# Performance work log

Measured on AMD Instinct MI355X. Metric: run time of the kernel, lower is better.

Reference implementation:

```python
import jax, jax.numpy as jnp
import numpy as np

B, Q, D, H, P, F = 16, 300, 256, 8, 4, 2048
HG = WG = 100          # feature-map height/width (hw = 10000, perfect square)
HW = HG * WG
DH = D // H
EPS = 1e-5


def _ln(x, g, b):
    m = x.mean(-1, keepdims=True)
    v = jnp.var(x, axis=-1, keepdims=True)
    return (x - m) * jax.lax.rsqrt(v + EPS) * g + b


def setup_inputs() -> dict:
    key = jax.random.key(0)
    ks = jax.random.split(key, 24)
    rn = lambda k, shape, s=0.02: jax.random.normal(k, shape, jnp.float32) * s
    return {
        "tgt": jax.random.normal(ks[0], (B, Q, D), jnp.float32),
        "memory": jax.random.normal(ks[1], (B, HW, D), jnp.float32),
        "in_proj_w": rn(ks[2], (D, 3 * D)), "in_proj_b": rn(ks[3], (3 * D,)),
        "out_proj_w": rn(ks[4], (D, D)), "out_proj_b": rn(ks[5], (D,)),
        "norm1_g": jnp.ones((D,), jnp.float32), "norm1_b": jnp.zeros((D,), jnp.float32),
        "ref_w": rn(ks[6], (D, 2)), "ref_b": rn(ks[7], (2,)),
        "off_w": rn(ks[8], (D, H * P * 2)), "off_b": rn(ks[9], (H * P * 2,)),
        "attw_w": rn(ks[10], (D, H * P)), "attw_b": rn(ks[11], (H * P,)),
        "vproj_w": rn(ks[12], (D, D)), "vproj_b": rn(ks[13], (D,)),
        "oproj_w": rn(ks[14], (D, D)), "oproj_b": rn(ks[15], (D,)),
        "norm2_g": jnp.ones((D,), jnp.float32), "norm2_b": jnp.zeros((D,), jnp.float32),
        "lin1_w": rn(ks[16], (D, F)), "lin1_b": rn(ks[17], (F,)),
        "lin2_w": rn(ks[18], (F, D)), "lin2_b": rn(ks[19], (D,)),
        "norm3_g": jnp.ones((D,), jnp.float32), "norm3_b": jnp.zeros((D,), jnp.float32),
    }


def reference(tgt, memory, in_proj_w, in_proj_b, out_proj_w, out_proj_b,
              norm1_g, norm1_b, ref_w, ref_b, off_w, off_b, attw_w, attw_b,
              vproj_w, vproj_b, oproj_w, oproj_b, norm2_g, norm2_b,
              lin1_w, lin1_b, lin2_w, lin2_b, norm3_g, norm3_b):
    # ---- self-attention (nn.MultiheadAttention, eval mode: dropout = identity)
    qkv = tgt @ in_proj_w + in_proj_b                      # [B,Q,3D]
    q, k, v = jnp.split(qkv, 3, axis=-1)
    q = q.reshape(B, Q, H, DH)
    k = k.reshape(B, Q, H, DH)
    v = v.reshape(B, Q, H, DH)
    scores = jnp.einsum('bqhd,bkhd->bhqk', q, k) / jnp.sqrt(jnp.float32(DH))
    attn = jax.nn.softmax(scores, axis=-1)
    sa = jnp.einsum('bhqk,bkhd->bqhd', attn, v).reshape(B, Q, D) @ out_proj_w + out_proj_b
    x = _ln(tgt + sa, norm1_g, norm1_b)

    # ---- reference points
    ref = jax.nn.sigmoid(x @ ref_w + ref_b)                # [B,Q,2] in (0,1)

    # ---- deformable cross-attention
    offs = (x @ off_w + off_b).reshape(B, Q, H, P, 2)
    wts = jax.nn.softmax((x @ attw_w + attw_b).reshape(B, Q, H, P), axis=-1)
    vals = (memory @ vproj_w + vproj_b).reshape(B, HW, H, DH)
    loc = jnp.clip(ref[:, :, None, None, :] + offs, 0.0, 1.0)
    sx = loc[..., 0] * (WG - 1)
    sy = loc[..., 1] * (HG - 1)
    x0 = jnp.floor(sx)
    y0 = jnp.floor(sy)
    x0i = jnp.clip(x0.astype(jnp.int32), 0, WG - 1)
    y0i = jnp.clip(y0.astype(jnp.int32), 0, HG - 1)
    x1i = jnp.clip(x0i + 1, 0, WG - 1)
    y1i = jnp.clip(y0i + 1, 0, HG - 1)
    wx1 = sx - x0
    wx0 = 1.0 - wx1
    wy1 = sy - y0
    wy0 = 1.0 - wy1
    bi = jnp.arange(B)[:, None, None, None]
    hi = jnp.arange(H)[None, None, :, None]

    def gather(yi, xi):                                    # [B,Q,H,P,DH]
        return vals[bi, yi * WG + xi, hi]

    samp = (gather(y0i, x0i) * (wx0 * wy0)[..., None]
            + gather(y1i, x0i) * (wx0 * wy1)[..., None]
            + gather(y0i, x1i) * (wx1 * wy0)[..., None]
            + gather(y1i, x1i) * (wx1 * wy1)[..., None])
    ca = (samp * wts[..., None]).sum(axis=3).reshape(B, Q, D) @ oproj_w + oproj_b
    x = _ln(x + ca, norm2_g, norm2_b)

    # ---- FFN
    ff = jax.nn.relu(x @ lin1_w + lin1_b) @ lin2_w + lin2_b
    return _ln(x + ff, norm3_g, norm3_b)
```

## Files before the change

### kernel.cpp

```cpp
#include <hip/hip_runtime.h>

#define NB   16
#define NQ   300
#define ND   256
#define NH   8
#define NP   4
#define NF   2048
#define NHW  10000
#define NWG  100
#define NROW 4800

typedef __attribute__((ext_vector_type(8))) short bf16x8;
typedef __attribute__((ext_vector_type(4))) float f32x4;

__device__ __forceinline__ unsigned short f2bf(float f) {
    unsigned u = __builtin_bit_cast(unsigned, f);
    u = (u + 0x7fffu + ((u >> 16) & 1u)) >> 16;
    return (unsigned short)u;
}
__device__ __forceinline__ float bf2f(unsigned short h) {
    unsigned u = ((unsigned)h) << 16;
    return __builtin_bit_cast(float, u);
}

__device__ __forceinline__ bf16x8 cvt8(float4 lo, float4 hi) {
    unsigned r0, r1, r2, r3;
    asm("v_cvt_pk_bf16_f32 %0, %1, %2" : "=v"(r0) : "v"(lo.x), "v"(lo.y));
    asm("v_cvt_pk_bf16_f32 %0, %1, %2" : "=v"(r1) : "v"(lo.z), "v"(lo.w));
    asm("v_cvt_pk_bf16_f32 %0, %1, %2" : "=v"(r2) : "v"(hi.x), "v"(hi.y));
    asm("v_cvt_pk_bf16_f32 %0, %1, %2" : "=v"(r3) : "v"(hi.z), "v"(hi.w));
    uint4 u = {r0, r1, r2, r3};
    return __builtin_bit_cast(bf16x8, u);
}

__device__ __forceinline__ void gl_lds16(const unsigned short* g, unsigned short* l) {
    __builtin_amdgcn_global_load_lds(
        (__attribute__((address_space(1))) const void*)g,
        (__attribute__((address_space(3))) void*)l,
        16, 0, 0);
}

__global__ __launch_bounds__(256) void transpose_cast(
    const float* __restrict__ w_in,  const float* __restrict__ w_out,
    const float* __restrict__ w_vp,  const float* __restrict__ w_op,
    const float* __restrict__ w_l1,  const float* __restrict__ w_l2,
    unsigned short* __restrict__ o_in, unsigned short* __restrict__ o_out,
    unsigned short* __restrict__ o_vp, unsigned short* __restrict__ o_op,
    unsigned short* __restrict__ o_l1, unsigned short* __restrict__ o_l2)
{
    __shared__ float ts[64][65];
    int b = blockIdx.x;
    const float* src; unsigned short* dst; int K, N, ncx;
    if      (b < 48)  { src = w_in;  dst = o_in;  K = 256;  N = 768;  ncx = 12; }
    else if (b < 64)  { src = w_out; dst = o_out; K = 256;  N = 256;  ncx = 4;  b -= 48; }
    else if (b < 80)  { src = w_vp;  dst = o_vp;  K = 256;  N = 256;  ncx = 4;  b -= 64; }
    else if (b < 96)  { src = w_op;  dst = o_op;  K = 256;  N = 256;  ncx = 4;  b -= 80; }
    else if (b < 224) { src = w_l1;  dst = o_l1;  K = 256;  N = 2048; ncx = 32; b -= 96; }
    else              { src = w_l2;  dst = o_l2;  K = 2048; N = 256;  ncx = 4;  b -= 224; }
    const int n0 = (b % ncx) * 64, k0 = (b / ncx) * 64;
    const int t = threadIdx.x;
    const int r = t >> 4, c = t & 15;
    #pragma unroll
    for (int j = 0; j < 4; j++) {
        float4 v = *(const float4*)(src + (long)(k0 + j * 16 + r) * N + n0 + c * 4);
        ts[j * 16 + r][c * 4 + 0] = v.x;
        ts[j * 16 + r][c * 4 + 1] = v.y;
        ts[j * 16 + r][c * 4 + 2] = v.z;
        ts[j * 16 + r][c * 4 + 3] = v.w;
    }
    __syncthreads();
    #pragma unroll
    for (int j = 0; j < 4; j++) {
        unsigned short o[4];
        #pragma unroll
        for (int i = 0; i < 4; i++)
            o[i] = f2bf(ts[c * 4 + i][j * 16 + r]);
        *(uint2*)(dst + (long)(n0 + j * 16 + r) * K + k0 + c * 4) = *(uint2*)o;
    }
}

__global__ __launch_bounds__(256) void prep_head(
    const float* __restrict__ rw, const float* __restrict__ rb,
    const float* __restrict__ ow, const float* __restrict__ ob,
    const float* __restrict__ aw, const float* __restrict__ ab,
    unsigned short* __restrict__ o_hd, float* __restrict__ o_hb)
{
    int id = blockIdx.x * 256 + threadIdx.x;
    if (id < 32768) {
        int n = id >> 8, k = id & 255;
        float v;
        if (n < 2)       v = rw[k * 2 + n];
        else if (n < 66) v = ow[k * 64 + (n - 2)];
        else if (n < 98) v = aw[k * 32 + (n - 66)];
        else             v = 0.0f;
        o_hd[id] = f2bf(v);
        return;
    }
    id -= 32768;
    if (id < 128) {
        float v;
        if (id < 2)       v = rb[id];
        else if (id < 66) v = ob[id - 2];
        else if (id < 98) v = ab[id - 66];
        else              v = 0.0f;
        o_hb[id] = v;
    }
}

template <int RELU, int OUTBF, int SPLITK, int TN>
__global__ __launch_bounds__(512, 4) void gemm_bt(
    const float* __restrict__ A, const unsigned short* __restrict__ Bt,
    const float* __restrict__ bias, void* __restrict__ Cout,
    int M, int N, int K)
{
    constexpr int NFB = TN / 16;
    constexpr int WN  = TN / 64;
    constexpr int AI  = WN;

    __shared__ __align__(16) unsigned short As[2][8 * 512];
    __shared__ __align__(16) unsigned short Bs[2][NFB * 512];

    const int t    = threadIdx.x;
    const long m0  = (long)blockIdx.y * 128;
    const int  n0  = blockIdx.x * TN;
    const int  wave = t >> 6, lane = t & 63;
    const int  l16 = lane & 15, quad = lane >> 4;
    const int  wmi = wave / WN, wni = wave % WN;
    const int  wm  = wmi * (AI * 16);
    const int  wn  = wni * 64;
    const int  fA  = wmi * AI;
    const int  fB  = wni * 4;

    f32x4 acc[AI][4] = {};

    const int kChunk = K / SPLITK;
    const int kBeg   = (SPLITK > 1) ? blockIdx.z * kChunk : 0;
    const int nk     = kChunk / 32;

    const long aRow   = m0 + wave * 16 + l16;
    const bool aValid = (aRow < M);
    const float* aP   = A + aRow * (long)K + kBeg + (quad << 3);
    unsigned short* aW = &As[0][(wave << 9) + (lane << 3)];

    const unsigned short* bP;
    unsigned short* bW;
    if constexpr (TN == 256) {
        bP = Bt + (long)(n0 + wave * 32 + l16) * K + kBeg + (quad << 3);
        bW = &Bs[0][wave << 10];
    } else {
        bP = Bt + (long)(n0 + wave * 16 + l16) * K + kBeg + (quad << 3);
        bW = &Bs[0][wave << 9];
    }

    float4 la0 = make_float4(0.f, 0.f, 0.f, 0.f);
    float4 la1 = make_float4(0.f, 0.f, 0.f, 0.f);

    auto loadA = [&](int kt) {
        if (aValid) {
            la0 = *(const float4*)(aP + kt * 32);
            la1 = *(const float4*)(aP + kt * 32 + 4);
        }
    };
    auto writeA = [&](int buf) {
        const bf16x8 v = cvt8(la0, la1);
        *(bf16x8*)(aW + buf * 4096) = v;
    };
    auto issueB = [&](int kt, int buf) {
        if constexpr (TN == 256) {
            gl_lds16(bP + kt * 32,          bW + buf * (NFB * 512));
            gl_lds16(bP + kt * 32 + 16 * (long)K, bW + buf * (NFB * 512) + 512);
        } else {
            gl_lds16(bP + kt * 32,          bW + buf * (NFB * 512));
        }
    };

    issueB(0, 0);
    loadA(0);
    writeA(0);
    __syncthreads();

    for (int kt = 0; kt < nk; kt++) {
        const int cur = kt & 1;
        if (kt + 1 < nk) {
            issueB(kt + 1, cur ^ 1);
            loadA(kt + 1);
        }

        bf16x8 af[AI], bfr[4];
        #pragma unroll
        for (int i = 0; i < AI; i++)
            af[i] = *(const bf16x8*)&As[cur][(fA + i) * 512 + (lane << 3)];
        #pragma unroll
        for (int j = 0; j < 4; j++)
            bfr[j] = *(const bf16x8*)&Bs[cur][(fB + j) * 512 + (lane << 3)];
        #pragma unroll
        for (int i = 0; i < AI; i++)
            #pragma unroll
            for (int j = 0; j < 4; j++)
                acc[i][j] = __builtin_amdgcn_mfma_f32_16x16x32_bf16(
                    bfr[j], af[i], acc[i][j], 0, 0, 0);

        if (kt + 1 < nk) {
            writeA(cur ^ 1);
            __syncthreads();
        }
    }

    float4 bj[4];
    #pragma unroll
    for (int j = 0; j < 4; j++)
        bj[j] = *(const float4*)&bias[n0 + wn + j * 16 + (quad << 2)];

    float* outp = (float*)Cout;
    float bscale = 1.0f;
    if (SPLITK > 1) {
        outp += (size_t)blockIdx.z * M * N;
        bscale = (blockIdx.z == 0) ? 1.0f : 0.0f;
    }

    #pragma unroll
    for (int i = 0; i < AI; i++) {
        const long gr = m0 + wm + i * 16 + l16;
        if (gr < M) {
            #pragma unroll
            for (int j = 0; j < 4; j++) {
                float4 v;
                v.x = acc[i][j][0] + bscale * bj[j].x;
                v.y = acc[i][j][1] + bscale * bj[j].y;
                v.z = acc[i][j][2] + bscale * bj[j].z;
                v.w = acc[i][j][3] + bscale * bj[j].w;
                if (RELU) {
                    v.x = fmaxf(v.x, 0.f); v.y = fmaxf(v.y, 0.f);
                    v.z = fmaxf(v.z, 0.f); v.w = fmaxf(v.w, 0.f);
                }
                const int gc = n0 + wn + j * 16 + (quad << 2);
                if (OUTBF) {
                    unsigned short o[4] = {f2bf(v.x), f2bf(v.y), f2bf(v.z), f2bf(v.w)};
                    *(uint2*)((unsigned short*)Cout + gr * N + gc) = *(uint2*)o;
                } else {
                    *(float4*)(outp + gr * N + gc) = v;
                }
            }
        }
    }
}

__global__ __launch_bounds__(256) void attn_kernel(
    const float* __restrict__ qkv, float* __restrict__ sa)
{
    __shared__ union {
        struct {
            unsigned short Ks[304][40];
            unsigned short Qs[64][40];
        } s;
        unsigned short Ps[4][16][328];
    } u;
    __shared__ unsigned short Vt[32][328];

    const int bh = blockIdx.y;
    const int b  = bh >> 3, h = bh & 7;
    const int q0 = blockIdx.x * 64;
    const int t  = threadIdx.x;

    for (int idx = t; idx < 304 * 8; idx += 256) {
        const int r = idx >> 3, c4 = (idx & 7) << 2;
        if (r < NQ) {
            const float4 kv = *(const float4*)(qkv + ((long)(b * NQ + r)) * 768 + 256 + h * 32 + c4);
            u.s.Ks[r][c4 + 0] = f2bf(kv.x); u.s.Ks[r][c4 + 1] = f2bf(kv.y);
            u.s.Ks[r][c4 + 2] = f2bf(kv.z); u.s.Ks[r][c4 + 3] = f2bf(kv.w);
        } else {
            u.s.Ks[r][c4 + 0] = 0; u.s.Ks[r][c4 + 1] = 0;
            u.s.Ks[r][c4 + 2] = 0; u.s.Ks[r][c4 + 3] = 0;
        }
    }
    for (int idx = t; idx < NQ * 8; idx += 256) {
        const int key = idx >> 3, dq = (idx & 7) << 2;
        const float4 vv = *(const float4*)(qkv + ((long)(b * NQ + key)) * 768 + 512 + h * 32 + dq);
        Vt[dq + 0][key] = f2bf(vv.x); Vt[dq + 1][key] = f2bf(vv.y);
        Vt[dq + 2][key] = f2bf(vv.z); Vt[dq + 3][key] = f2bf(vv.w);
    }
    for (int idx = t; idx < 32 * 20; idx += 256)
        Vt[idx / 20][300 + idx % 20] = 0;
    for (int idx = t; idx < 64 * 8; idx += 256) {
        const int r = idx >> 3, c4 = (idx & 7) << 2;
        const int q = q0 + r;
        if (q < NQ) {
            const float4 qv = *(const float4*)(qkv + ((long)(b * NQ + q)) * 768 + h * 32 + c4);
            u.s.Qs[r][c4 + 0] = f2bf(qv.x); u.s.Qs[r][c4 + 1] = f2bf(qv.y);
            u.s.Qs[r][c4 + 2] = f2bf(qv.z); u.s.Qs[r][c4 + 3] = f2bf(qv.w);
        } else {
            u.s.Qs[r][c4 + 0] = 0; u.s.Qs[r][c4 + 1] = 0;
            u.s.Qs[r][c4 + 2] = 0; u.s.Qs[r][c4 + 3] = 0;
        }
    }
    __syncthreads();

    const int wave = t >> 6, lane = t & 63;
    const int l16 = lane & 15, quad = lane >> 4;
    const float scale = 0.1767766952966369f;

    const bf16x8 aq = *(const bf16x8*)&u.s.Qs[wave * 16 + l16][quad * 8];
    f32x4 sacc[19];
    #pragma unroll
    for (int kt = 0; kt < 19; kt++) {
        const bf16x8 bk = *(const bf16x8*)&u.s.Ks[kt * 16 + l16][quad * 8];
        sacc[kt] = __builtin_amdgcn_mfma_f32_16x16x32_bf16(
            aq, bk, (f32x4){0.f, 0.f, 0.f, 0.f}, 0, 0, 0);
    }

    float inv[4];
    #pragma unroll
    for (int r = 0; r < 4; r++) {
        float m = -1e30f;
        #pragma unroll
        for (int kt = 0; kt < 19; kt++) {
            float s = sacc[kt][r] * scale;
            if (kt == 18 && l16 >= 12) s = -1e30f;
            sacc[kt][r] = s;
            m = fmaxf(m, s);
        }
        m = fmaxf(m, __shfl_xor(m, 1)); m = fmaxf(m, __shfl_xor(m, 2));
        m = fmaxf(m, __shfl_xor(m, 4)); m = fmaxf(m, __shfl_xor(m, 8));
        float sum = 0.f;
        #pragma unroll
        for (int kt = 0; kt < 19; kt++) {
            float p = __expf(sacc[kt][r] - m);
            sacc[kt][r] = p;
            sum += p;
        }
        sum += __shfl_xor(sum, 1); sum += __shfl_xor(sum, 2);
        sum += __shfl_xor(sum, 4); sum += __shfl_xor(sum, 8);
        inv[r] = 1.0f / sum;
    }

    __syncthreads();

    #pragma unroll
    for (int kt = 0; kt < 19; kt++)
        #pragma unroll
        for (int r = 0; r < 4; r++)
            u.Ps[wave][quad * 4 + r][kt * 16 + l16] = f2bf(sacc[kt][r] * inv[r]);
    #pragma unroll
    for (int r = 0; r < 4; r++)
        u.Ps[wave][quad * 4 + r][304 + l16] = 0;

    f32x4 o0 = {0.f, 0.f, 0.f, 0.f}, o1 = {0.f, 0.f, 0.f, 0.f};
    #pragma unroll
    for (int kt = 0; kt < 10; kt++) {
        const bf16x8 ap  = *(const bf16x8*)&u.Ps[wave][l16][kt * 32 + quad * 8];
        const bf16x8 bv0 = *(const bf16x8*)&Vt[l16][kt * 32 + quad * 8];
        const bf16x8 bv1 = *(const bf16x8*)&Vt[16 + l16][kt * 32 + quad * 8];
        o0 = __builtin_amdgcn_mfma_f32_16x16x32_bf16(ap, bv0, o0, 0, 0, 0);
        o1 = __builtin_amdgcn_mfma_f32_16x16x32_bf16(ap, bv1, o1, 0, 0, 0);
    }

    #pragma unroll
    for (int r = 0; r < 4; r++) {
        const int q = q0 + wave * 16 + quad * 4 + r;
        if (q < NQ) {
            float* op = sa + ((long)(b * NQ + q)) * ND + h * 32;
            op[l16]      = o0[r];
            op[16 + l16] = o1[r];
        }
    }
}

template <int NPART>
__global__ __launch_bounds__(256) void residual_ln(
    const float* __restrict__ a, const float* __restrict__ r,
    const float* __restrict__ gam, const float* __restrict__ bet,
    float* __restrict__ out, long pstride)
{
    const int row  = blockIdx.x * 4 + (threadIdx.x >> 6);
    const int lane = threadIdx.x & 63;
    const long base = (long)row * ND + lane * 4;
    float4 av = *(const float4*)(a + base);
    float4 rv = *(const float4*)(r + base);
    #pragma unroll
    for (int z = 1; z < NPART; z++) {
        float4 pv = *(const float4*)(r + z * pstride + base);
        rv.x += pv.x; rv.y += pv.y; rv.z += pv.z; rv.w += pv.w;
    }
    float x0 = av.x + rv.x, x1 = av.y + rv.y, x2 = av.z + rv.z, x3 = av.w + rv.w;
    float s  = x0 + x1 + x2 + x3;
    float s2 = x0 * x0 + x1 * x1 + x2 * x2 + x3 * x3;
    #pragma unroll
    for (int off = 32; off >= 1; off >>= 1) {
        s  += __shfl_xor(s, off);
        s2 += __shfl_xor(s2, off);
    }
    float mean = s * 0.00390625f;
    float var  = s2 * 0.00390625f - mean * mean;
    float rstd = rsqrtf(var + 1e-5f);
    float4 gv = *(const float4*)(gam + lane * 4);
    float4 bv = *(const float4*)(bet + lane * 4);
    float4 o;
    o.x = (x0 - mean) * rstd * gv.x + bv.x;
    o.y = (x1 - mean) * rstd * gv.y + bv.y;
    o.z = (x2 - mean) * rstd * gv.z + bv.z;
    o.w = (x3 - mean) * rstd * gv.w + bv.w;
    *(float4*)(out + base) = o;
}

__global__ __launch_bounds__(256) void meta_kernel(
    const float* __restrict__ res, float* __restrict__ meta)
{
    const int t   = threadIdx.x;
    const int row = blockIdx.x * 8 + (t >> 5);
    const int s   = t & 31;
    const int h   = s >> 2;
    const float* rp = res + (long)row * 128;
    const float rx = 1.f / (1.f + __expf(-rp[0]));
    const float ry = 1.f / (1.f + __expf(-rp[1]));
    const float offx = rp[2 + 2 * s], offy = rp[3 + 2 * s];
    const float a0 = rp[66 + h * 4 + 0], a1 = rp[66 + h * 4 + 1];
    const float a2 = rp[66 + h * 4 + 2], a3 = rp[66 + h * 4 + 3];
    const float mx = fmaxf(fmaxf(a0, a1), fmaxf(a2, a3));
    const float den = __expf(a0 - mx) + __expf(a1 - mx) +
                      __expf(a2 - mx) + __expf(a3 - mx);
    const float awt = __expf(rp[66 + s] - mx) / den;

    const float lx = fminf(fmaxf(rx + offx, 0.f), 1.f) * (NWG - 1);
    const float ly = fminf(fmaxf(ry + offy, 0.f), 1.f) * (NWG - 1);
    const float fx = floorf(lx), fy = floorf(ly);
    int x0 = (int)fx; x0 = min(max(x0, 0), NWG - 1);
    int y0 = (int)fy; y0 = min(max(y0, 0), NWG - 1);
    const int x1 = min(x0 + 1, NWG - 1);
    const int y1 = min(y0 + 1, NWG - 1);
    const float wx1 = lx - fx, wx0 = 1.f - wx1;
    const float wy1 = ly - fy, wy0 = 1.f - wy1;
    float4 m0, m1;
    m0.x = __int_as_float(y0 * NWG + x0);
    m0.y = __int_as_float(y0 * NWG + x1);
    m0.z = __int_as_float(y1 * NWG + x0);
    m0.w = __int_as_float(y1 * NWG + x1);
    m1.x = awt * wx0 * wy0;
    m1.y = awt * wx1 * wy0;
    m1.z = awt * wx0 * wy1;
    m1.w = awt * wx1 * wy1;
    float* mp = meta + (long)row * 256 + s * 8;
    *(float4*)mp       = m0;
    *(float4*)(mp + 4) = m1;
}

__global__ __launch_bounds__(256) void deform_gather(
    const float* __restrict__ meta, const unsigned short* __restrict__ vals,
    float* __restrict__ ca)
{
    const int row = blockIdx.x;
    const int b = row / NQ;
    __shared__ float ms[256];
    const int t = threadIdx.x;
    ms[t] = meta[(long)row * 256 + t];
    __syncthreads();
    const int h = t >> 5, d = t & 31;
    const unsigned short* vb = vals + (long)b * NHW * ND + h * 32 + d;
    float acc = 0.f;
    #pragma unroll
    for (int p = 0; p < NP; p++) {
        const float* mp = ms + h * 32 + p * 8;
        const int i00 = __float_as_int(mp[0]);
        const int i01 = __float_as_int(mp[1]);
        const int i10 = __float_as_int(mp[2]);
        const int i11 = __float_as_int(mp[3]);
        acc += mp[4] * bf2f(vb[(long)i00 * ND]);
        acc += mp[5] * bf2f(vb[(long)i01 * ND]);
        acc += mp[6] * bf2f(vb[(long)i10 * ND]);
        acc += mp[7] * bf2f(vb[(long)i11 * ND]);
    }
    ca[(long)row * ND + t] = acc;
}

extern "C" void kernel_launch(void* const* d_in, const int* in_sizes, int n_in,
                              void* d_out, int out_size, void* d_ws, size_t ws_size,
                              hipStream_t stream)
{
    (void)in_sizes; (void)n_in; (void)out_size; (void)ws_size;
    const float* tgt   = (const float*)d_in[0];
    const float* mem   = (const float*)d_in[1];
    const float* inpw  = (const float*)d_in[2];
    const float* inpb  = (const float*)d_in[3];
    const float* outw  = (const float*)d_in[4];
    const float* outb  = (const float*)d_in[5];
    const float* n1g   = (const float*)d_in[6];
    const float* n1b   = (const float*)d_in[7];
    const float* refw  = (const float*)d_in[8];
    const float* refb  = (const float*)d_in[9];
    const float* offw  = (const float*)d_in[10];
    const float* offb  = (const float*)d_in[11];
    const float* attww = (const float*)d_in[12];
    const float* attwb = (const float*)d_in[13];
    const float* vpw   = (const float*)d_in[14];
    const float* vpb   = (const float*)d_in[15];
    const float* opw   = (const float*)d_in[16];
    const float* opb   = (const float*)d_in[17];
    const float* n2g   = (const float*)d_in[18];
    const float* n2b   = (const float*)d_in[19];
    const float* l1w   = (const float*)d_in[20];
    const float* l1b   = (const float*)d_in[21];
    const float* l2w   = (const float*)d_in[22];
    const float* l2b   = (const float*)d_in[23];
    const float* n3g   = (const float*)d_in[24];
    const float* n3b   = (const float*)d_in[25];
    float* out = (float*)d_out;

    char* p = (char*)d_ws;
    auto alloc = [&](size_t bytes) {
        char* r = p; p += (bytes + 255) & ~(size_t)255; return (void*)r;
    };
    unsigned short* wtIn   = (unsigned short*)alloc(768 * 256 * 2);
    unsigned short* wtOut  = (unsigned short*)alloc(256 * 256 * 2);
    unsigned short* wtVp   = (unsigned short*)alloc(256 * 256 * 2);
    unsigned short* wtOp   = (unsigned short*)alloc(256 * 256 * 2);
    unsigned short* wtL1   = (unsigned short*)alloc(2048 * 256 * 2);
    unsigned short* wtL2   = (unsigned short*)alloc(256 * 2048 * 2);
    unsigned short* wtHead = (unsigned short*)alloc(128 * 256 * 2);
    float*          headb  = (float*)alloc(128 * 4);
    float* qkv  = (float*)alloc((size_t)NROW * 768 * 4);
    float* sa   = (float*)alloc((size_t)NROW * ND * 4);
    float* x1   = (float*)alloc((size_t)NROW * ND * 4);
    float* x2   = (float*)alloc((size_t)NROW * ND * 4);
    float* tmp  = (float*)alloc((size_t)NROW * ND * 4 * 4);
    float* ca   = (float*)alloc((size_t)NROW * ND * 4);
    float* meta = (float*)alloc((size_t)NROW * 256 * 4);
    void* uni = alloc((size_t)NB * NHW * ND * 2);
    unsigned short* vals = (unsigned short*)uni;
    float* h1 = (float*)uni;
    float* res = qkv;

    transpose_cast<<<352, 256, 0, stream>>>(
        inpw, outw, vpw, opw, l1w, l2w,
        wtIn, wtOut, wtVp, wtOp, wtL1, wtL2);
    prep_head<<<129, 256, 0, stream>>>(refw, refb, offw, offb, attww, attwb,
                                       wtHead, headb);

    gemm_bt<0, 0, 1, 256><<<dim3(3, 38), 512, 0, stream>>>(tgt, wtIn, inpb, qkv,
                                                           NROW, 768, 256);
    gemm_bt<0, 1, 1, 256><<<dim3(1, 1250), 512, 0, stream>>>(mem, wtVp, vpb, vals,
                                                             NB * NHW, 256, 256);
    attn_kernel<<<dim3(5, 128), 256, 0, stream>>>(qkv, sa);
    gemm_bt<0, 0, 1, 256><<<dim3(1, 38), 512, 0, stream>>>(sa, wtOut, outb, tmp,
                                                           NROW, 256, 256);
    residual_ln<1><<<1200, 256, 0, stream>>>(tgt, tmp, n1g, n1b, x1, 0);
    gemm_bt<0, 0, 1, 128><<<dim3(1, 38), 512, 0, stream>>>(x1, wtHead, headb, res,
                                                           NROW, 128, 256);
    meta_kernel<<<600, 256, 0, stream>>>(res, meta);
    deform_gather<<<4800, 256, 0, stream>>>(meta, vals, ca);
    gemm_bt<0, 0, 1, 256><<<dim3(1, 38), 512, 0, stream>>>(ca, wtOp, opb, tmp,
                                                           NROW, 256, 256);
    residual_ln<1><<<1200, 256, 0, stream>>>(x1, tmp, n2g, n2b, x2, 0);
    gemm_bt<1, 0, 1, 256><<<dim3(8, 38), 512, 0, stream>>>(x2, wtL1, l1b, h1,
                                                           NROW, 2048, 256);
    gemm_bt<0, 0, 4, 256><<<dim3(1, 38, 4), 512, 0, stream>>>(h1, wtL2, l2b, tmp,
                                                              NROW, 256, 2048);
    residual_ln<4><<<1200, 256, 0, stream>>>(x2, tmp, n3g, n3b, out,
                                             (long)NROW * 256);
}
```

Baseline: 499.0 us.

## Add persistent value-projection GEMM with LDS-resident weights and register double-buffered A

Replaces the generic tiled GEMM for the large memory value projection (160000x256x256) with a dedicated kernel. Each block loads the whole 256x256 bf16 weight into LDS once, then streams 640 rows of A through registers in a two-slot double buffer, running MFMA directly from register-converted A fragments. This removes the per-k-tile B reloads, the A staging through LDS and the per-tile syncs of the old kernel. In exchange it needs 128KB of LDS and many registers per block, which lowers occupancy, and it runs only 250 blocks.

New measurement: 520.0 us. +4.2%, slower.

```diff
diff --git a/kernel.cpp b/kernel.cpp
--- a/kernel.cpp
+++ b/kernel.cpp
@@ -107,6 +107,88 @@
     }
 }
 
+__global__ __launch_bounds__(512, 2) void gemm_vproj_bs(
+    const float* __restrict__ A, const unsigned short* __restrict__ Bt,
+    const float* __restrict__ bias, unsigned short* __restrict__ Cout)
+{
+    __shared__ __align__(16) unsigned short Bs[128 * 512];
+
+    const int t    = threadIdx.x;
+    const int wave = t >> 6, lane = t & 63;
+    const int l16  = lane & 15, quad = lane >> 4;
+    const int wmi  = wave >> 2, wni = wave & 3;
+    const long m0  = (long)blockIdx.x * 640;
+
+    {
+        const unsigned short* bp = Bt + (long)(wave * 32 + l16) * 256 + (quad << 3);
+        unsigned short* bw = &Bs[wave << 13];
+        #pragma unroll
+        for (int kf = 0; kf < 8; kf++) {
+            gl_lds16(bp + kf * 32,            bw + kf * 512);
+            gl_lds16(bp + kf * 32 + 16 * 256, bw + 4096 + kf * 512);
+        }
+    }
+    __syncthreads();
+
+    float4 bj[4];
+    #pragma unroll
+    for (int j = 0; j < 4; j++)
+        bj[j] = *(const float4*)&bias[wni * 64 + j * 16 + (quad << 2)];
+
+    const float* aBase = A + (m0 + wmi * 16 + l16) * 256L + (quad << 3);
+
+    float4 xa[16], ya[16];
+
+    auto loadX = [&](int it) {
+        const float* ap = aBase + (long)it * 32 * 256;
+        #pragma unroll
+        for (int kf = 0; kf < 8; kf++) {
+            xa[2 * kf]     = *(const float4*)(ap + kf * 32);
+            xa[2 * kf + 1] = *(const float4*)(ap + kf * 32 + 4);
+        }
+    };
+    auto loadY = [&](int it) {
+        const float* ap = aBase + (long)it * 32 * 256;
+        #pragma unroll
+        for (int kf = 0; kf < 8; kf++) {
+            ya[2 * kf]     = *(const float4*)(ap + kf * 32);
+            ya[2 * kf + 1] = *(const float4*)(ap + kf * 32 + 4);
+        }
+    };
+    auto computeStore = [&](const float4* a, int it) {
+        f32x4 acc[4] = {};
+        #pragma unroll
+        for (int kf = 0; kf < 8; kf++) {
+            const bf16x8 af = cvt8(a[2 * kf], a[2 * kf + 1]);
+            #pragma unroll
+            for (int j = 0; j < 4; j++) {
+                const bf16x8 bv = *(const bf16x8*)
+                    &Bs[((wni * 4 + j) * 8 + kf) * 512 + (lane << 3)];
+                acc[j] = __builtin_amdgcn_mfma_f32_16x16x32_bf16(
+                    bv, af, acc[j], 0, 0, 0);
+            }
+        }
+        const long gr = m0 + it * 32 + wmi * 16 + l16;
+        #pragma unroll
+        for (int j = 0; j < 4; j++) {
+            unsigned short o[4] = {f2bf(acc[j][0] + bj[j].x),
+                                   f2bf(acc[j][1] + bj[j].y),
+                                   f2bf(acc[j][2] + bj[j].z),
+                                   f2bf(acc[j][3] + bj[j].w)};
+            const int gc = wni * 64 + j * 16 + (quad << 2);
+            *(uint2*)(Cout + gr * 256 + gc) = *(uint2*)o;
+        }
+    };
+
+    loadX(0);
+    for (int it = 0; it < 20; it += 2) {
+        loadY(it + 1);
+        computeStore(xa, it);
+        if (it + 2 < 20) loadX(it + 2);
+        computeStore(ya, it + 1);
+    }
+}
+
 template <int RELU, int OUTBF, int SPLITK, int TN>
 __global__ __launch_bounds__(512, 4) void gemm_bt(
     const float* __restrict__ A, const unsigned short* __restrict__ Bt,
@@ -167,10 +249,10 @@
     };
     auto issueB = [&](int kt, int buf) {
         if constexpr (TN == 256) {
-            gl_lds16(bP + kt * 32,          bW + buf * (NFB * 512));
+            gl_lds16(bP + kt * 32,                bW + buf * (NFB * 512));
             gl_lds16(bP + kt * 32 + 16 * (long)K, bW + buf * (NFB * 512) + 512);
         } else {
-            gl_lds16(bP + kt * 32,          bW + buf * (NFB * 512));
+            gl_lds16(bP + kt * 32,                bW + buf * (NFB * 512));
         }
     };
 
@@ -536,8 +618,7 @@
 
     gemm_bt<0, 0, 1, 256><<<dim3(3, 38), 512, 0, stream>>>(tgt, wtIn, inpb, qkv,
                                                            NROW, 768, 256);
-    gemm_bt<0, 1, 1, 256><<<dim3(1, 1250), 512, 0, stream>>>(mem, wtVp, vpb, vals,
-                                                             NB * NHW, 256, 256);
+    gemm_vproj_bs<<<250, 512, 0, stream>>>(mem, wtVp, vpb, vals);
     attn_kernel<<<dim3(5, 128), 256, 0, stream>>>(qkv, sa);
     gemm_bt<0, 0, 1, 256><<<dim3(1, 38), 512, 0, stream>>>(sa, wtOut, outb, tmp,
                                                            NROW, 256, 256);
```

## Add dedicated value-projection GEMM with LDS-resident weights and register double-buffered A

Applied to the files above, without the earlier changes.

Replaces the generic tiled GEMM for the large memory value projection (160000x256x256) with a specialized kernel. Each block loads the whole bf16 weight matrix into 128KB of LDS once, then streams 640 rows of fp32 A directly into registers, double-buffered across 32-row iterations, converting to bf16 in registers and feeding MFMA without staging A through LDS. This is meant to cut repeated B tile loads, LDS traffic for A and per-k-step synchronisation in this memory-bound GEMM. In exchange it uses heavy register and LDS footprint, which limits occupancy to about one or two blocks per CU, and it launches 250 blocks.

Measured after the change: 509.1 us. +2.0%, slower.

```diff
diff --git a/kernel.cpp b/kernel.cpp
--- a/kernel.cpp
+++ b/kernel.cpp
@@ -107,6 +107,100 @@
     }
 }
 
+#define VLD(V, ap)                                  \
+    V##0  = *(const float4*)((ap));                 \
+    V##1  = *(const float4*)((ap) + 4);             \
+    V##2  = *(const float4*)((ap) + 32);            \
+    V##3  = *(const float4*)((ap) + 36);            \
+    V##4  = *(const float4*)((ap) + 64);            \
+    V##5  = *(const float4*)((ap) + 68);            \
+    V##6  = *(const float4*)((ap) + 96);            \
+    V##7  = *(const float4*)((ap) + 100);           \
+    V##8  = *(const float4*)((ap) + 128);           \
+    V##9  = *(const float4*)((ap) + 132);           \
+    V##10 = *(const float4*)((ap) + 160);           \
+    V##11 = *(const float4*)((ap) + 164);           \
+    V##12 = *(const float4*)((ap) + 192);           \
+    V##13 = *(const float4*)((ap) + 196);           \
+    V##14 = *(const float4*)((ap) + 224);           \
+    V##15 = *(const float4*)((ap) + 228);
+
+#define VKF(V, a, b, kf)                                                      \
+    {   const bf16x8 af = cvt8(V##a, V##b);                                   \
+        const bf16x8 bv0 = *(const bf16x8*)(bsBase + (0 * 8 + kf) * 512);     \
+        const bf16x8 bv1 = *(const bf16x8*)(bsBase + (1 * 8 + kf) * 512);     \
+        const bf16x8 bv2 = *(const bf16x8*)(bsBase + (2 * 8 + kf) * 512);     \
+        const bf16x8 bv3 = *(const bf16x8*)(bsBase + (3 * 8 + kf) * 512);     \
+        acc0 = __builtin_amdgcn_mfma_f32_16x16x32_bf16(bv0, af, acc0, 0, 0, 0); \
+        acc1 = __builtin_amdgcn_mfma_f32_16x16x32_bf16(bv1, af, acc1, 0, 0, 0); \
+        acc2 = __builtin_amdgcn_mfma_f32_16x16x32_bf16(bv2, af, acc2, 0, 0, 0); \
+        acc3 = __builtin_amdgcn_mfma_f32_16x16x32_bf16(bv3, af, acc3, 0, 0, 0); }
+
+#define STORE1(acc, bj, off)                                                  \
+    {   unsigned short o[4] = {f2bf(acc[0] + bj.x), f2bf(acc[1] + bj.y),      \
+                               f2bf(acc[2] + bj.z), f2bf(acc[3] + bj.w)};     \
+        *(uint2*)(cp + (off)) = *(uint2*)o; }
+
+#define VCOMP(V, it)                                                          \
+    {   f32x4 acc0 = {0.f, 0.f, 0.f, 0.f}, acc1 = {0.f, 0.f, 0.f, 0.f};      \
+        f32x4 acc2 = {0.f, 0.f, 0.f, 0.f}, acc3 = {0.f, 0.f, 0.f, 0.f};      \
+        VKF(V, 0, 1, 0)   VKF(V, 2, 3, 1)   VKF(V, 4, 5, 2)   VKF(V, 6, 7, 3) \
+        VKF(V, 8, 9, 4)   VKF(V, 10, 11, 5) VKF(V, 12, 13, 6) VKF(V, 14, 15, 7) \
+        const long gr = m0 + (long)(it) * 32 + wmi * 16 + l16;                \
+        unsigned short* cp = Cout + gr * 256 + wni * 64 + (quad << 2);        \
+        STORE1(acc0, bj0, 0)  STORE1(acc1, bj1, 16)                           \
+        STORE1(acc2, bj2, 32) STORE1(acc3, bj3, 48) }
+
+__global__ __launch_bounds__(512, 2) void gemm_vproj_bs(
+    const float* __restrict__ A, const unsigned short* __restrict__ Bt,
+    const float* __restrict__ bias, unsigned short* __restrict__ Cout)
+{
+    __shared__ __align__(16) unsigned short Bs[128 * 512];
+
+    const int t    = threadIdx.x;
+    const int wave = t >> 6, lane = t & 63;
+    const int l16  = lane & 15, quad = lane >> 4;
+    const int wmi  = wave >> 2, wni = wave & 3;
+    const long m0  = (long)blockIdx.x * 640;
+
+    {
+        const unsigned short* bp = Bt + (long)(wave * 32 + l16) * 256 + (quad << 3);
+        unsigned short* bw = &Bs[wave << 13];
+        #pragma unroll
+        for (int kf = 0; kf < 8; kf++) {
+            gl_lds16(bp + kf * 32,            bw + kf * 512);
+            gl_lds16(bp + kf * 32 + 16 * 256, bw + 4096 + kf * 512);
+        }
+    }
+    __syncthreads();
+
+    float4 bj0 = *(const float4*)&bias[wni * 64 +  0 + (quad << 2)];
+    float4 bj1 = *(const float4*)&bias[wni * 64 + 16 + (quad << 2)];
+    float4 bj2 = *(const float4*)&bias[wni * 64 + 32 + (quad << 2)];
+    float4 bj3 = *(const float4*)&bias[wni * 64 + 48 + (quad << 2)];
+
+    const float* aBase = A + (m0 + wmi * 16 + l16) * 256L + (quad << 3);
+    const unsigned short* bsBase = &Bs[(wni * 32) * 512 + (lane << 3)];
+
+    float4 x0, x1, x2, x3, x4, x5, x6, x7, x8, x9, x10, x11, x12, x13, x14, x15;
+    float4 y0, y1, y2, y3, y4, y5, y6, y7, y8, y9, y10, y11, y12, y13, y14, y15;
+
+    VLD(x, aBase)
+    __builtin_amdgcn_sched_barrier(0);
+    for (int it = 0; it < 20; it += 2) {
+        const float* apY = aBase + (long)(it + 1) * 8192;
+        VLD(y, apY)
+        __builtin_amdgcn_sched_barrier(0);
+        VCOMP(x, it)
+        if (it + 2 < 20) {
+            const float* apX = aBase + (long)(it + 2) * 8192;
+            VLD(x, apX)
+            __builtin_amdgcn_sched_barrier(0);
+        }
+        VCOMP(y, it + 1)
+    }
+}
+
 template <int RELU, int OUTBF, int SPLITK, int TN>
 __global__ __launch_bounds__(512, 4) void gemm_bt(
     const float* __restrict__ A, const unsigned short* __restrict__ Bt,
@@ -167,10 +261,10 @@
     };
     auto issueB = [&](int kt, int buf) {
         if constexpr (TN == 256) {
-            gl_lds16(bP + kt * 32,          bW + buf * (NFB * 512));
+            gl_lds16(bP + kt * 32,                bW + buf * (NFB * 512));
             gl_lds16(bP + kt * 32 + 16 * (long)K, bW + buf * (NFB * 512) + 512);
         } else {
-            gl_lds16(bP + kt * 32,          bW + buf * (NFB * 512));
+            gl_lds16(bP + kt * 32,                bW + buf * (NFB * 512));
         }
     };
 
@@ -536,8 +630,7 @@
 
     gemm_bt<0, 0, 1, 256><<<dim3(3, 38), 512, 0, stream>>>(tgt, wtIn, inpb, qkv,
                                                            NROW, 768, 256);
-    gemm_bt<0, 1, 1, 256><<<dim3(1, 1250), 512, 0, stream>>>(mem, wtVp, vpb, vals,
-                                                             NB * NHW, 256, 256);
+    gemm_vproj_bs<<<250, 512, 0, stream>>>(mem, wtVp, vpb, vals);
     attn_kernel<<<dim3(5, 128), 256, 0, stream>>>(qkv, sa);
     gemm_bt<0, 0, 1, 256><<<dim3(1, 38), 512, 0, stream>>>(sa, wtOut, outb, tmp,
                                                            NROW, 256, 256);
```

## Add B-stationary value-projection GEMM and split-K the small output-projection GEMMs

Applied to the files above, without the earlier changes.

Adds a dedicated value-projection GEMM kernel. It loads the whole 256x256 bf16 weight into LDS once per block, then streams 40 row tiles of 16 fp32 activation rows through double-buffered global-to-LDS loads, converting them to bf16 just before the MFMA. This is meant to stop the weight tile being reloaded for every 128-row block in the largest GEMM, which reads all of memory, and to cut the launch to 250 blocks. Separately, the two 256x256 output-projection GEMMs now use split-K 2 with a 2-way-summing residual LN to raise block count on small grids, at the cost of extra partial-sum traffic. The new kernel uses 128KB+ of LDS per block, which limits occupancy, and relies on hand-placed vmcnt waits.

After: 480.6 us. 1.04x faster.

```diff
diff --git a/kernel.cpp b/kernel.cpp
--- a/kernel.cpp
+++ b/kernel.cpp
@@ -34,6 +34,12 @@
 }
 
 __device__ __forceinline__ void gl_lds16(const unsigned short* g, unsigned short* l) {
+    __builtin_amdgcn_global_load_lds(
+        (__attribute__((address_space(1))) const void*)g,
+        (__attribute__((address_space(3))) void*)l,
+        16, 0, 0);
+}
+__device__ __forceinline__ void gl_lds16f(const float* g, float* l) {
     __builtin_amdgcn_global_load_lds(
         (__attribute__((address_space(1))) const void*)g,
         (__attribute__((address_space(3))) void*)l,
@@ -107,6 +113,83 @@
     }
 }
 
+__global__ __launch_bounds__(512, 2) void gemm_vproj_bs(
+    const float* __restrict__ A, const unsigned short* __restrict__ Bt,
+    const float* __restrict__ bias, unsigned short* __restrict__ Cout)
+{
+    __shared__ __align__(16) unsigned short Bs[128 * 512];
+    __shared__ __align__(16) float As[2][16 * 256];
+
+    const int t    = threadIdx.x;
+    const int wave = t >> 6, lane = t & 63;
+    const int l16  = lane & 15, quad = lane >> 4;
+    const long m0  = (long)blockIdx.x * 640;
+
+    {
+        const unsigned short* bp = Bt + (long)(wave * 32 + l16) * 256 + (quad << 3);
+        unsigned short* bw = &Bs[wave << 13];
+        #pragma unroll
+        for (int kf = 0; kf < 8; kf++) {
+            gl_lds16(bp + kf * 32,            bw + kf * 512);
+            gl_lds16(bp + kf * 32 + 16 * 256, bw + 4096 + kf * 512);
+        }
+    }
+
+    const float* aG = A + (m0 + l16) * 256 + wave * 32 + (quad << 3);
+    auto issueA = [&](int it, int buf) {
+        const float* g = aG + (long)it * 16 * 256;
+        gl_lds16f(g,     &As[buf][wave * 512]);
+        gl_lds16f(g + 4, &As[buf][wave * 512 + 256]);
+    };
+
+    issueA(0, 0);
+    __syncthreads();
+
+    float4 bj0 = *(const float4*)&bias[wave * 32 + (quad << 2)];
+    float4 bj1 = *(const float4*)&bias[wave * 32 + 16 + (quad << 2)];
+
+    const unsigned short* bF0 = &Bs[(wave << 13)] + (lane << 3);
+    const unsigned short* bF1 = bF0 + 4096;
+
+    for (int it = 0; it < 40; ++it) {
+        const int cur = it & 1;
+        if (it + 1 < 40) {
+            issueA(it + 1, cur ^ 1);
+            asm volatile("s_waitcnt vmcnt(2)" ::: "memory");
+        } else {
+            asm volatile("s_waitcnt vmcnt(0)" ::: "memory");
+        }
+        __builtin_amdgcn_sched_barrier(0);
+
+        f32x4 acc0 = {0.f, 0.f, 0.f, 0.f}, acc1 = {0.f, 0.f, 0.f, 0.f};
+        #pragma unroll
+        for (int kf = 0; kf < 8; kf++) {
+            const float4 alo = *(const float4*)&As[cur][kf * 512 + (lane << 2)];
+            const float4 ahi = *(const float4*)&As[cur][kf * 512 + 256 + (lane << 2)];
+            const bf16x8 af  = cvt8(alo, ahi);
+            const bf16x8 bv0 = *(const bf16x8*)(bF0 + kf * 512);
+            const bf16x8 bv1 = *(const bf16x8*)(bF1 + kf * 512);
+            acc0 = __builtin_amdgcn_mfma_f32_16x16x32_bf16(bv0, af, acc0, 0, 0, 0);
+            acc1 = __builtin_amdgcn_mfma_f32_16x16x32_bf16(bv1, af, acc1, 0, 0, 0);
+        }
+
+        const long gr = m0 + (long)it * 16 + l16;
+        unsigned short* cp = Cout + gr * 256 + wave * 32 + (quad << 2);
+        {
+            unsigned short o[4] = {f2bf(acc0[0] + bj0.x), f2bf(acc0[1] + bj0.y),
+                                   f2bf(acc0[2] + bj0.z), f2bf(acc0[3] + bj0.w)};
+            *(uint2*)cp = *(uint2*)o;
+        }
+        {
+            unsigned short o[4] = {f2bf(acc1[0] + bj1.x), f2bf(acc1[1] + bj1.y),
+                                   f2bf(acc1[2] + bj1.z), f2bf(acc1[3] + bj1.w)};
+            *(uint2*)(cp + 16) = *(uint2*)o;
+        }
+
+        __builtin_amdgcn_s_barrier();
+    }
+}
+
 template <int RELU, int OUTBF, int SPLITK, int TN>
 __global__ __launch_bounds__(512, 4) void gemm_bt(
     const float* __restrict__ A, const unsigned short* __restrict__ Bt,
@@ -167,10 +250,10 @@
     };
     auto issueB = [&](int kt, int buf) {
         if constexpr (TN == 256) {
-            gl_lds16(bP + kt * 32,          bW + buf * (NFB * 512));
+            gl_lds16(bP + kt * 32,                bW + buf * (NFB * 512));
             gl_lds16(bP + kt * 32 + 16 * (long)K, bW + buf * (NFB * 512) + 512);
         } else {
-            gl_lds16(bP + kt * 32,          bW + buf * (NFB * 512));
+            gl_lds16(bP + kt * 32,                bW + buf * (NFB * 512));
         }
     };
 
@@ -536,19 +619,20 @@
 
     gemm_bt<0, 0, 1, 256><<<dim3(3, 38), 512, 0, stream>>>(tgt, wtIn, inpb, qkv,
                                                            NROW, 768, 256);
-    gemm_bt<0, 1, 1, 256><<<dim3(1, 1250), 512, 0, stream>>>(mem, wtVp, vpb, vals,
-                                                             NB * NHW, 256, 256);
+    gemm_vproj_bs<<<250, 512, 0, stream>>>(mem, wtVp, vpb, vals);
     attn_kernel<<<dim3(5, 128), 256, 0, stream>>>(qkv, sa);
-    gemm_bt<0, 0, 1, 256><<<dim3(1, 38), 512, 0, stream>>>(sa, wtOut, outb, tmp,
-                                                           NROW, 256, 256);
-    residual_ln<1><<<1200, 256, 0, stream>>>(tgt, tmp, n1g, n1b, x1, 0);
+    gemm_bt<0, 0, 2, 256><<<dim3(1, 38, 2), 512, 0, stream>>>(sa, wtOut, outb, tmp,
+                                                              NROW, 256, 256);
+    residual_ln<2><<<1200, 256, 0, stream>>>(tgt, tmp, n1g, n1b, x1,
+                                             (long)NROW * 256);
     gemm_bt<0, 0, 1, 128><<<dim3(1, 38), 512, 0, stream>>>(x1, wtHead, headb, res,
                                                            NROW, 128, 256);
     meta_kernel<<<600, 256, 0, stream>>>(res, meta);
     deform_gather<<<4800, 256, 0, stream>>>(meta, vals, ca);
-    gemm_bt<0, 0, 1, 256><<<dim3(1, 38), 512, 0, stream>>>(ca, wtOp, opb, tmp,
-                                                           NROW, 256, 256);
-    residual_ln<1><<<1200, 256, 0, stream>>>(x1, tmp, n2g, n2b, x2, 0);
+    gemm_bt<0, 0, 2, 256><<<dim3(1, 38, 2), 512, 0, stream>>>(ca, wtOp, opb, tmp,
+                                                              NROW, 256, 256);
+    residual_ln<2><<<1200, 256, 0, stream>>>(x1, tmp, n2g, n2b, x2,
+                                             (long)NROW * 256);
     gemm_bt<1, 0, 1, 256><<<dim3(8, 38), 512, 0, stream>>>(x2, wtL1, l1b, h1,
                                                            NROW, 2048, 256);
     gemm_bt<0, 0, 4, 256><<<dim3(1, 38, 4), 512, 0, stream>>>(h1, wtL2, l2b, tmp,
```
